# Optimization experiments

Hardware: AMD Instinct MI355X
Metric: run time of the kernel (lower is better)

## Reference

```python
import jax, jax.numpy as jnp
import numpy as np

HEADS = 4
DIM_HEAD = 32


def setup_inputs() -> dict:
    key = jax.random.key(0)
    k1, k2, k3 = jax.random.split(key, 3)
    B, L, D = 16, 8192, 256
    hidden = HEADS * DIM_HEAD  # 128
    x = jax.random.normal(k1, (B, L, D), dtype=jnp.float32)
    W_qkv = jax.random.normal(k2, (D, 3 * hidden), dtype=jnp.float32) * (D ** -0.5)
    W_out = jax.random.normal(k3, (hidden, D), dtype=jnp.float32) * (hidden ** -0.5)
    b_out = jnp.zeros((D,), dtype=jnp.float32)
    return {"x": x, "W_qkv": W_qkv, "W_out": W_out, "b_out": b_out}


def reference(x, W_qkv, W_out, b_out):
    B, L, D = x.shape
    scale = DIM_HEAD ** -0.5
    # 1x1 conv == per-token matmul
    qkv = jnp.einsum('bld,df->blf', x, W_qkv)  # [B, L, 3*h*dh]
    qkv = qkv.reshape(B, L, 3, HEADS, DIM_HEAD)
    q = jnp.transpose(qkv[:, :, 0], (0, 2, 1, 3)) * scale          # [B, h, L, d]
    k = jax.nn.softmax(jnp.transpose(qkv[:, :, 1], (0, 2, 1, 3)), axis=2)  # softmax over L
    v = jnp.transpose(qkv[:, :, 2], (0, 2, 1, 3))                  # [B, h, L, e]
    context = jnp.einsum('bhld,bhle->bhde', k, v)                  # [B, h, d, e]
    out = jnp.einsum('bhde,bhld->bhle', context, q)                # [B, h, L, e]
    out = jnp.transpose(out, (0, 2, 1, 3)).reshape(B, L, HEADS * DIM_HEAD)
    return jnp.einsum('blf,fd->bld', out, W_out) + b_out
```

## Files before the change

### kernel.cpp

```cpp
#include <hip/hip_runtime.h>
#include <math.h>


typedef __attribute__((ext_vector_type(8))) short bf16x8;
typedef __attribute__((ext_vector_type(4))) float f32x4;
typedef __attribute__((ext_vector_type(4))) unsigned u32x4;

__device__ __forceinline__ unsigned cvt_pk2(float a, float b) {
    unsigned r;
    asm("v_cvt_pk_bf16_f32 %0, %1, %2" : "=v"(r) : "v"(a), "v"(b));
    return r;
}
__device__ __forceinline__ ushort bf16_rn(float f) {
    return (ushort)cvt_pk2(f, f);
}
__device__ __forceinline__ float bf16f(ushort h) { return __uint_as_float(((unsigned)h) << 16); }

__device__ __forceinline__ void glds16(const void* g, void* l) {
    __builtin_amdgcn_global_load_lds((const __attribute__((address_space(1))) unsigned int*)g,
                                     (__attribute__((address_space(3))) unsigned int*)l,
                                     16, 0, 0);
}

__global__ __launch_bounds__(256) void prep_kernel(const float* __restrict__ W,
                                                   ushort* __restrict__ wh,
                                                   ushort* __restrict__ wl) {
    int n = blockIdx.x, k = threadIdx.x;
    float f = W[k * 384 + 128 + n];
    ushort h = bf16_rn(f);
    wh[n * 256 + k] = h;
    wl[n * 256 + k] = bf16_rn(f - bf16f(h));
}

__global__ __launch_bounds__(256) void gemm_kv(
    const float* __restrict__ X,
    const ushort* __restrict__ Wh, const ushort* __restrict__ Wl,
    float* __restrict__ S_part, float* __restrict__ Z_part) {
    __shared__ __align__(16) char smem[40960];
    float*  As  = (float*)smem;
    ushort* Bsh = (ushort*)(smem + 8192);
    ushort* Bsl = (ushort*)(smem + 8192 + 16384);
    float*  tile = (float*)smem;

    const int tid = threadIdx.x;
    const int blk = blockIdx.x;
    const long row0 = (long)blk * 64;
    const int lane = tid & 63, wave = tid >> 6;
    const int wc = wave * 64;
    const int m = lane & 15, quad = lane >> 4;
    const int ra = lane >> 3, pa = lane & 7;
    const int rb = lane >> 2, pb = lane & 3;

    f32x4 acc[4][4] = {};

    for (int k0 = 0; k0 < 256; k0 += 32) {
#pragma unroll
        for (int s = 0; s < 2; ++s) {
            int seg = s * 4 + wave;
            int r = seg * 8 + ra;
            int q = pa ^ (r & 7);
            glds16(&X[(row0 + r) * 256 + k0 + q * 4], &As[seg * 256]);
        }
#pragma unroll
        for (int s = 0; s < 4; ++s) {
            int seg = s * 4 + wave;
            int r = seg * 16 + rb;
            int q = pb ^ ((r >> 1) & 3);
            glds16(&Wh[r * 256 + k0 + q * 8], &Bsh[seg * 512]);
            glds16(&Wl[r * 256 + k0 + q * 8], &Bsl[seg * 512]);
        }
        __syncthreads();

        bf16x8 bh[4], bl[4];
#pragma unroll
        for (int j = 0; j < 4; ++j) {
            int r = wc + j * 16 + m;
            int p = quad ^ ((r >> 1) & 3);
            bh[j] = *(const bf16x8*)&Bsh[r * 32 + p * 8];
            bl[j] = *(const bf16x8*)&Bsl[r * 32 + p * 8];
        }
#pragma unroll
        for (int i = 0; i < 4; ++i) {
            int r = i * 16 + m;
            int p0 = (quad * 2) ^ (r & 7);
            int p1 = (quad * 2 + 1) ^ (r & 7);
            f32x4 a0 = *(const f32x4*)&As[r * 32 + p0 * 4];
            f32x4 a1 = *(const f32x4*)&As[r * 32 + p1 * 4];
            u32x4 ahw, alw;
#pragma unroll
            for (int e = 0; e < 2; ++e) {
                float f0 = a0[2 * e], f1 = a0[2 * e + 1];
                unsigned h = cvt_pk2(f0, f1);
                ahw[e] = h;
                alw[e] = cvt_pk2(f0 - __uint_as_float(h << 16),
                                 f1 - __uint_as_float(h & 0xFFFF0000u));
            }
#pragma unroll
            for (int e = 0; e < 2; ++e) {
                float f0 = a1[2 * e], f1 = a1[2 * e + 1];
                unsigned h = cvt_pk2(f0, f1);
                ahw[2 + e] = h;
                alw[2 + e] = cvt_pk2(f0 - __uint_as_float(h << 16),
                                     f1 - __uint_as_float(h & 0xFFFF0000u));
            }
            bf16x8 ah = __builtin_bit_cast(bf16x8, ahw);
            bf16x8 al = __builtin_bit_cast(bf16x8, alw);
#pragma unroll
            for (int j = 0; j < 4; ++j) {
                acc[i][j] = __builtin_amdgcn_mfma_f32_16x16x32_bf16(ah, bh[j], acc[i][j], 0, 0, 0);
                acc[i][j] = __builtin_amdgcn_mfma_f32_16x16x32_bf16(ah, bl[j], acc[i][j], 0, 0, 0);
                acc[i][j] = __builtin_amdgcn_mfma_f32_16x16x32_bf16(al, bh[j], acc[i][j], 0, 0, 0);
            }
        }
        __syncthreads();
    }

    const int h = wave, d = lane >> 1, eg = lane & 1, e0 = eg * 16;
    float sacc[16] = {};
    float z = 0.f;
    for (int half = 0; half < 2; ++half) {
        if (half) __syncthreads();
#pragma unroll
        for (int ii = 0; ii < 2; ++ii) {
            int i = half * 2 + ii;
#pragma unroll
            for (int r4 = 0; r4 < 4; ++r4) {
                int rl = ii * 16 + quad * 4 + r4;
#pragma unroll
                for (int j = 0; j < 4; ++j) {
                    int c = wc + j * 16 + m;
                    float v = acc[i][j][r4];
                    tile[rl * 260 + c] = (c < 128) ? __expf(v) : v;
                }
            }
        }
        __syncthreads();
#pragma unroll 4
        for (int l = 0; l < 32; ++l) {
            const float* rowp = &tile[l * 260];
            float ek = rowp[h * 32 + d];
            const f32x4* vp = (const f32x4*)&rowp[128 + h * 32 + e0];
            f32x4 v0 = vp[0], v1 = vp[1], v2 = vp[2], v3 = vp[3];
            z += ek;
            sacc[0]  += ek * v0[0]; sacc[1]  += ek * v0[1]; sacc[2]  += ek * v0[2]; sacc[3]  += ek * v0[3];
            sacc[4]  += ek * v1[0]; sacc[5]  += ek * v1[1]; sacc[6]  += ek * v1[2]; sacc[7]  += ek * v1[3];
            sacc[8]  += ek * v2[0]; sacc[9]  += ek * v2[1]; sacc[10] += ek * v2[2]; sacc[11] += ek * v2[3];
            sacc[12] += ek * v3[0]; sacc[13] += ek * v3[1]; sacc[14] += ek * v3[2]; sacc[15] += ek * v3[3];
        }
    }
    long sb = (long)blk * 4096 + h * 1024 + d * 32 + e0;
#pragma unroll
    for (int t = 0; t < 16; ++t) S_part[sb + t] = sacc[t];
    if (eg == 0) Z_part[blk * 128 + h * 32 + d] = z;
}

__global__ __launch_bounds__(256) void reduce_parts(const float* __restrict__ Sp,
                                                    const float* __restrict__ Zp,
                                                    float* __restrict__ S,
                                                    float* __restrict__ Z) {
    int g = blockIdx.x * 256 + threadIdx.x;
    int b = g >> 12, idx = g & 4095;
    const float* p = Sp + ((long)b * 128) * 4096 + idx;
    float s0 = 0.f, s1 = 0.f;
#pragma unroll 4
    for (int j = 0; j < 64; ++j) { s0 += p[j * 4096]; s1 += p[(j + 64) * 4096]; }
    S[g] = s0 + s1;
    if (g < 2048) {
        int bb = g >> 7, c = g & 127;
        const float* q = Zp + (long)bb * 128 * 128 + c;
        float z0 = 0.f, z1 = 0.f;
#pragma unroll 4
        for (int j = 0; j < 64; ++j) { z0 += q[j * 128]; z1 += q[(j + 64) * 128]; }
        Z[g] = z0 + z1;
    }
}

__global__ __launch_bounds__(256) void combine_kernel(const float* __restrict__ S,
                                                      const float* __restrict__ Z,
                                                      const float* __restrict__ Wout,
                                                      float* __restrict__ m2f) {
    int bh = blockIdx.x;
    int b = bh >> 2, h = bh & 3;
    int n = threadIdx.x;
    __shared__ float ctx[32][33];
    __shared__ float zs[32];
    if (n < 32) zs[n] = Z[b * 128 + h * 32 + n];
    __syncthreads();
#pragma unroll
    for (int t = 0; t < 4; ++t) {
        int idx = t * 256 + n;
        ctx[idx >> 5][idx & 31] = S[(long)b * 4096 + h * 1024 + idx] / zs[idx >> 5];
    }
    __syncthreads();
    const float scale = 0.17677669529663687f;
    float acc[32];
#pragma unroll
    for (int dd = 0; dd < 32; ++dd) acc[dd] = 0.f;
    for (int e = 0; e < 32; ++e) {
        float w = Wout[(h * 32 + e) * 256 + n];
#pragma unroll
        for (int dd = 0; dd < 32; ++dd) acc[dd] += ctx[dd][e] * w;
    }
#pragma unroll
    for (int dd = 0; dd < 32; ++dd)
        m2f[((long)(b * 128 + h * 32 + dd)) * 256 + n] = acc[dd] * scale;
}

__global__ __launch_bounds__(256) void w2eff_kernel(const float* __restrict__ Wqkv,
                                                    const float* __restrict__ m2f,
                                                    ushort* __restrict__ w2h,
                                                    ushort* __restrict__ w2l) {
    int bid = blockIdx.x;
    int b = bid >> 4, kg = bid & 15;
    int n = threadIdx.x;
    __shared__ float lWq[16 * 128];
#pragma unroll
    for (int u = 0; u < 8; ++u) {
        int idx = u * 256 + n;
        int k = idx >> 7, hd = idx & 127;
        lWq[idx] = Wqkv[(kg * 16 + k) * 384 + hd];
    }
    __syncthreads();
    float acc[16] = {};
    for (int hd = 0; hd < 128; ++hd) {
        float mm = m2f[((long)(b * 128 + hd)) * 256 + n];
#pragma unroll
        for (int k = 0; k < 16; ++k) acc[k] += lWq[k * 128 + hd] * mm;
    }
    long base = ((long)(b * 256 + n)) * 256 + kg * 16;
#pragma unroll
    for (int k = 0; k < 16; ++k) {
        ushort hh = bf16_rn(acc[k]);
        w2h[base + k] = hh;
        w2l[base + k] = bf16_rn(acc[k] - bf16f(hh));
    }
}

__global__ __launch_bounds__(256) void gemm2_kernel(
    const float* __restrict__ X,
    const ushort* __restrict__ W2h, const ushort* __restrict__ W2l,
    const float* __restrict__ bias, float* __restrict__ out) {
    __shared__ __align__(16) float  As[4096];
    __shared__ __align__(16) ushort Bsh[4096];
    __shared__ __align__(16) ushort Bsl[4096];
    const int tid = threadIdx.x;
    const int wg = blockIdx.x;
    const int xcd = wg & 7;
    const int u = wg >> 3;
    const int cbl = u & 1;
    const int gid = (u >> 1) * 8 + xcd;
    const long bz = gid >> 6;
    const int row0 = (gid & 63) * 128;
    const int col0 = cbl * 128;
    const float* Xb = X + bz * (8192L * 256);
    const ushort* Bh = W2h + bz * (256L * 256);
    const ushort* Bl = W2l + bz * (256L * 256);
    const int lane = tid & 63, wave = tid >> 6;
    const int wr = (wave & 1) * 64, wc = (wave >> 1) * 64;
    const int m = lane & 15, quad = lane >> 4;
    const int ra = lane >> 3, pa = lane & 7;
    const int rb = lane >> 2, pb = lane & 3;

    f32x4 acc[4][4] = {};

    for (int k0 = 0; k0 < 256; k0 += 32) {
#pragma unroll
        for (int s = 0; s < 4; ++s) {
            int seg = s * 4 + wave;
            int r = seg * 8 + ra;
            int q = pa ^ (r & 7);
            glds16(&Xb[(long)(row0 + r) * 256 + k0 + q * 4], &As[seg * 256]);
        }
#pragma unroll
        for (int s = 0; s < 2; ++s) {
            int seg = s * 4 + wave;
            int r = seg * 16 + rb;
            int q = pb ^ ((r >> 1) & 3);
            glds16(&Bh[(col0 + r) * 256 + k0 + q * 8], &Bsh[seg * 512]);
            glds16(&Bl[(col0 + r) * 256 + k0 + q * 8], &Bsl[seg * 512]);
        }
        __syncthreads();

        bf16x8 bh[4], bl[4];
#pragma unroll
        for (int j = 0; j < 4; ++j) {
            int r = wc + j * 16 + m;
            int p = quad ^ ((r >> 1) & 3);
            bh[j] = *(const bf16x8*)&Bsh[r * 32 + p * 8];
            bl[j] = *(const bf16x8*)&Bsl[r * 32 + p * 8];
        }
#pragma unroll
        for (int i = 0; i < 4; ++i) {
            int r = wr + i * 16 + m;
            int p0 = (quad * 2) ^ (r & 7);
            int p1 = (quad * 2 + 1) ^ (r & 7);
            f32x4 a0 = *(const f32x4*)&As[r * 32 + p0 * 4];
            f32x4 a1 = *(const f32x4*)&As[r * 32 + p1 * 4];
            u32x4 ahw, alw;
#pragma unroll
            for (int e = 0; e < 2; ++e) {
                float f0 = a0[2 * e], f1 = a0[2 * e + 1];
                unsigned h = cvt_pk2(f0, f1);
                ahw[e] = h;
                alw[e] = cvt_pk2(f0 - __uint_as_float(h << 16),
                                 f1 - __uint_as_float(h & 0xFFFF0000u));
            }
#pragma unroll
            for (int e = 0; e < 2; ++e) {
                float f0 = a1[2 * e], f1 = a1[2 * e + 1];
                unsigned h = cvt_pk2(f0, f1);
                ahw[2 + e] = h;
                alw[2 + e] = cvt_pk2(f0 - __uint_as_float(h << 16),
                                     f1 - __uint_as_float(h & 0xFFFF0000u));
            }
            bf16x8 ah = __builtin_bit_cast(bf16x8, ahw);
            bf16x8 al = __builtin_bit_cast(bf16x8, alw);
#pragma unroll
            for (int j = 0; j < 4; ++j) {
                acc[i][j] = __builtin_amdgcn_mfma_f32_16x16x32_bf16(ah, bh[j], acc[i][j], 0, 0, 0);
                acc[i][j] = __builtin_amdgcn_mfma_f32_16x16x32_bf16(ah, bl[j], acc[i][j], 0, 0, 0);
                acc[i][j] = __builtin_amdgcn_mfma_f32_16x16x32_bf16(al, bh[j], acc[i][j], 0, 0, 0);
            }
        }
        __syncthreads();
    }

    float bv[4];
#pragma unroll
    for (int j = 0; j < 4; ++j) bv[j] = bias[col0 + wc + j * 16 + m];
    float* outb = out + bz * (8192L * 256);
#pragma unroll
    for (int i = 0; i < 4; ++i)
#pragma unroll
        for (int r4 = 0; r4 < 4; ++r4) {
            long row = row0 + wr + i * 16 + quad * 4 + r4;
#pragma unroll
            for (int j = 0; j < 4; ++j)
                outb[row * 256 + col0 + wc + j * 16 + m] = acc[i][j][r4] + bv[j];
        }
}

extern "C" void kernel_launch(void* const* d_in, const int* in_sizes, int n_in,
                              void* d_out, int out_size, void* d_ws, size_t ws_size,
                              hipStream_t stream) {
    const float* x     = (const float*)d_in[0];
    const float* W_qkv = (const float*)d_in[1];
    const float* W_out = (const float*)d_in[2];
    const float* b_out = (const float*)d_in[3];
    float* out = (float*)d_out;

    char* p = (char*)d_ws;
    ushort* wth = (ushort*)p; p += 256 * 256 * 2;
    ushort* wtl = (ushort*)p; p += 256 * 256 * 2;
    float* Sp   = (float*)p;  p += (long)2048 * 4096 * 4;
    float* Zp   = (float*)p;  p += 2048 * 128 * 4;
    float* Sr   = (float*)p;  p += 16 * 4096 * 4;
    float* Zr   = (float*)p;  p += 2048 * 4;
    float* m2f  = (float*)p;  p += 16 * 128 * 256 * 4;
    ushort* w2h = (ushort*)p; p += (long)16 * 256 * 256 * 2;
    ushort* w2l = (ushort*)p; p += (long)16 * 256 * 256 * 2;

    prep_kernel<<<256, 256, 0, stream>>>(W_qkv, wth, wtl);
    gemm_kv<<<2048, 256, 0, stream>>>(x, wth, wtl, Sp, Zp);
    reduce_parts<<<256, 256, 0, stream>>>(Sp, Zp, Sr, Zr);
    combine_kernel<<<64, 256, 0, stream>>>(Sr, Zr, W_out, m2f);
    w2eff_kernel<<<256, 256, 0, stream>>>(W_qkv, m2f, w2h, w2l);
    gemm2_kernel<<<2048, 256, 0, stream>>>(x, w2h, w2l, b_out, out);
}
```

Measured before the change: 388.5 us.

## Use single bf16 pass for K/V GEMM and pre-split X once in LDS

The K/V projection GEMM drops the three-pass split-bf16 scheme and uses one plain bf16 MFMA pass, so the low-part weight buffer and its prep are removed. X is loaded into registers, converted to bf16, and written to LDS in bf16 form. In the output GEMM, X is split into hi/lo bf16 once per tile while staging into LDS, instead of every wave re-converting the fp32 fragments it reads. This cuts MFMA count and conversion work, but the K/V path now carries bf16 rounding error into the softmax over L and the context.

```diff
diff --git a/kernel.cpp b/kernel.cpp
--- a/kernel.cpp
+++ b/kernel.cpp
@@ -23,23 +23,18 @@
 }
 
 __global__ __launch_bounds__(256) void prep_kernel(const float* __restrict__ W,
-                                                   ushort* __restrict__ wh,
-                                                   ushort* __restrict__ wl) {
+                                                   ushort* __restrict__ wh) {
     int n = blockIdx.x, k = threadIdx.x;
-    float f = W[k * 384 + 128 + n];
-    ushort h = bf16_rn(f);
-    wh[n * 256 + k] = h;
-    wl[n * 256 + k] = bf16_rn(f - bf16f(h));
+    wh[n * 256 + k] = bf16_rn(W[k * 384 + 128 + n]);
 }
 
 __global__ __launch_bounds__(256) void gemm_kv(
     const float* __restrict__ X,
-    const ushort* __restrict__ Wh, const ushort* __restrict__ Wl,
+    const ushort* __restrict__ Wh,
     float* __restrict__ S_part, float* __restrict__ Z_part) {
-    __shared__ __align__(16) char smem[40960];
-    float*  As  = (float*)smem;
-    ushort* Bsh = (ushort*)(smem + 8192);
-    ushort* Bsl = (ushort*)(smem + 8192 + 16384);
+    __shared__ __align__(16) char smem[33280];
+    ushort* Ash = (ushort*)smem;
+    ushort* Bsh = (ushort*)(smem + 4096);
     float*  tile = (float*)smem;
 
     const int tid = threadIdx.x;
@@ -48,70 +43,47 @@
     const int lane = tid & 63, wave = tid >> 6;
     const int wc = wave * 64;
     const int m = lane & 15, quad = lane >> 4;
-    const int ra = lane >> 3, pa = lane & 7;
     const int rb = lane >> 2, pb = lane & 3;
+    const int rA = tid >> 2, qA = tid & 3;
+    const int pA = qA ^ ((rA >> 1) & 3);
 
     f32x4 acc[4][4] = {};
 
     for (int k0 = 0; k0 < 256; k0 += 32) {
-#pragma unroll
-        for (int s = 0; s < 2; ++s) {
-            int seg = s * 4 + wave;
-            int r = seg * 8 + ra;
-            int q = pa ^ (r & 7);
-            glds16(&X[(row0 + r) * 256 + k0 + q * 4], &As[seg * 256]);
-        }
+        const float* xp = &X[(row0 + rA) * 256 + k0 + qA * 8];
+        f32x4 x0 = *(const f32x4*)xp;
+        f32x4 x1 = *(const f32x4*)(xp + 4);
 #pragma unroll
         for (int s = 0; s < 4; ++s) {
             int seg = s * 4 + wave;
             int r = seg * 16 + rb;
             int q = pb ^ ((r >> 1) & 3);
             glds16(&Wh[r * 256 + k0 + q * 8], &Bsh[seg * 512]);
-            glds16(&Wl[r * 256 + k0 + q * 8], &Bsl[seg * 512]);
-        }
-        __syncthreads();
-
-        bf16x8 bh[4], bl[4];
+        }
+        u32x4 aw;
+        aw[0] = cvt_pk2(x0[0], x0[1]); aw[1] = cvt_pk2(x0[2], x0[3]);
+        aw[2] = cvt_pk2(x1[0], x1[1]); aw[3] = cvt_pk2(x1[2], x1[3]);
+        *(u32x4*)&Ash[rA * 32 + pA * 8] = aw;
+        __syncthreads();
+
+        bf16x8 bh[4], av[4];
 #pragma unroll
         for (int j = 0; j < 4; ++j) {
             int r = wc + j * 16 + m;
             int p = quad ^ ((r >> 1) & 3);
             bh[j] = *(const bf16x8*)&Bsh[r * 32 + p * 8];
-            bl[j] = *(const bf16x8*)&Bsl[r * 32 + p * 8];
         }
 #pragma unroll
         for (int i = 0; i < 4; ++i) {
             int r = i * 16 + m;
-            int p0 = (quad * 2) ^ (r & 7);
-            int p1 = (quad * 2 + 1) ^ (r & 7);
-            f32x4 a0 = *(const f32x4*)&As[r * 32 + p0 * 4];
-            f32x4 a1 = *(const f32x4*)&As[r * 32 + p1 * 4];
-            u32x4 ahw, alw;
-#pragma unroll
-            for (int e = 0; e < 2; ++e) {
-                float f0 = a0[2 * e], f1 = a0[2 * e + 1];
-                unsigned h = cvt_pk2(f0, f1);
-                ahw[e] = h;
-                alw[e] = cvt_pk2(f0 - __uint_as_float(h << 16),
-                                 f1 - __uint_as_float(h & 0xFFFF0000u));
-            }
-#pragma unroll
-            for (int e = 0; e < 2; ++e) {
-                float f0 = a1[2 * e], f1 = a1[2 * e + 1];
-                unsigned h = cvt_pk2(f0, f1);
-                ahw[2 + e] = h;
-                alw[2 + e] = cvt_pk2(f0 - __uint_as_float(h << 16),
-                                     f1 - __uint_as_float(h & 0xFFFF0000u));
-            }
-            bf16x8 ah = __builtin_bit_cast(bf16x8, ahw);
-            bf16x8 al = __builtin_bit_cast(bf16x8, alw);
-#pragma unroll
-            for (int j = 0; j < 4; ++j) {
-                acc[i][j] = __builtin_amdgcn_mfma_f32_16x16x32_bf16(ah, bh[j], acc[i][j], 0, 0, 0);
-                acc[i][j] = __builtin_amdgcn_mfma_f32_16x16x32_bf16(ah, bl[j], acc[i][j], 0, 0, 0);
-                acc[i][j] = __builtin_amdgcn_mfma_f32_16x16x32_bf16(al, bh[j], acc[i][j], 0, 0, 0);
-            }
-        }
+            int p = quad ^ ((r >> 1) & 3);
+            av[i] = *(const bf16x8*)&Ash[r * 32 + p * 8];
+        }
+#pragma unroll
+        for (int i = 0; i < 4; ++i)
+#pragma unroll
+            for (int j = 0; j < 4; ++j)
+                acc[i][j] = __builtin_amdgcn_mfma_f32_16x16x32_bf16(av[i], bh[j], acc[i][j], 0, 0, 0);
         __syncthreads();
     }
 
@@ -240,7 +212,8 @@
     const float* __restrict__ X,
     const ushort* __restrict__ W2h, const ushort* __restrict__ W2l,
     const float* __restrict__ bias, float* __restrict__ out) {
-    __shared__ __align__(16) float  As[4096];
+    __shared__ __align__(16) ushort Ash[4096];
+    __shared__ __align__(16) ushort Asl[4096];
     __shared__ __align__(16) ushort Bsh[4096];
     __shared__ __align__(16) ushort Bsl[4096];
     const int tid = threadIdx.x;
@@ -258,18 +231,19 @@
     const int lane = tid & 63, wave = tid >> 6;
     const int wr = (wave & 1) * 64, wc = (wave >> 1) * 64;
     const int m = lane & 15, quad = lane >> 4;
-    const int ra = lane >> 3, pa = lane & 7;
     const int rb = lane >> 2, pb = lane & 3;
 
     f32x4 acc[4][4] = {};
 
     for (int k0 = 0; k0 < 256; k0 += 32) {
-#pragma unroll
-        for (int s = 0; s < 4; ++s) {
-            int seg = s * 4 + wave;
-            int r = seg * 8 + ra;
-            int q = pa ^ (r & 7);
-            glds16(&Xb[(long)(row0 + r) * 256 + k0 + q * 4], &As[seg * 256]);
+        f32x4 xv[2][2];
+#pragma unroll
+        for (int t = 0; t < 2; ++t) {
+            int uu = t * 256 + tid;
+            int r = uu >> 2, q = uu & 3;
+            const float* xp = &Xb[(long)(row0 + r) * 256 + k0 + q * 8];
+            xv[t][0] = *(const f32x4*)xp;
+            xv[t][1] = *(const f32x4*)(xp + 4);
         }
 #pragma unroll
         for (int s = 0; s < 2; ++s) {
@@ -279,49 +253,53 @@
             glds16(&Bh[(col0 + r) * 256 + k0 + q * 8], &Bsh[seg * 512]);
             glds16(&Bl[(col0 + r) * 256 + k0 + q * 8], &Bsl[seg * 512]);
         }
-        __syncthreads();
-
-        bf16x8 bh[4], bl[4];
-#pragma unroll
-        for (int j = 0; j < 4; ++j) {
-            int r = wc + j * 16 + m;
-            int p = quad ^ ((r >> 1) & 3);
-            bh[j] = *(const bf16x8*)&Bsh[r * 32 + p * 8];
-            bl[j] = *(const bf16x8*)&Bsl[r * 32 + p * 8];
-        }
+#pragma unroll
+        for (int t = 0; t < 2; ++t) {
+            int uu = t * 256 + tid;
+            int r = uu >> 2, q = uu & 3;
+            int p = q ^ ((r >> 1) & 3);
+            u32x4 hw, lw;
+#pragma unroll
+            for (int e = 0; e < 2; ++e) {
+                float f0 = xv[t][0][2 * e], f1 = xv[t][0][2 * e + 1];
+                unsigned hh = cvt_pk2(f0, f1);
+                hw[e] = hh;
+                lw[e] = cvt_pk2(f0 - __uint_as_float(hh << 16),
+                                f1 - __uint_as_float(hh & 0xFFFF0000u));
+            }
+#pragma unroll
+            for (int e = 0; e < 2; ++e) {
+                float f0 = xv[t][1][2 * e], f1 = xv[t][1][2 * e + 1];
+                unsigned hh = cvt_pk2(f0, f1);
+                hw[2 + e] = hh;
+                lw[2 + e] = cvt_pk2(f0 - __uint_as_float(hh << 16),
+                                    f1 - __uint_as_float(hh & 0xFFFF0000u));
+            }
+            *(u32x4*)&Ash[r * 32 + p * 8] = hw;
+            *(u32x4*)&Asl[r * 32 + p * 8] = lw;
+        }
+        __syncthreads();
+
+        bf16x8 af[2][4], bg[2][4];
 #pragma unroll
         for (int i = 0; i < 4; ++i) {
-            int r = wr + i * 16 + m;
-            int p0 = (quad * 2) ^ (r & 7);
-            int p1 = (quad * 2 + 1) ^ (r & 7);
-            f32x4 a0 = *(const f32x4*)&As[r * 32 + p0 * 4];
-            f32x4 a1 = *(const f32x4*)&As[r * 32 + p1 * 4];
-            u32x4 ahw, alw;
-#pragma unroll
-            for (int e = 0; e < 2; ++e) {
-                float f0 = a0[2 * e], f1 = a0[2 * e + 1];
-                unsigned h = cvt_pk2(f0, f1);
-                ahw[e] = h;
-                alw[e] = cvt_pk2(f0 - __uint_as_float(h << 16),
-                                 f1 - __uint_as_float(h & 0xFFFF0000u));
+            int rA = wr + i * 16 + m;
+            int pA = quad ^ ((rA >> 1) & 3);
+            af[0][i] = *(const bf16x8*)&Ash[rA * 32 + pA * 8];
+            af[1][i] = *(const bf16x8*)&Asl[rA * 32 + pA * 8];
+            int rB = wc + i * 16 + m;
+            int pB = quad ^ ((rB >> 1) & 3);
+            bg[0][i] = *(const bf16x8*)&Bsh[rB * 32 + pB * 8];
+            bg[1][i] = *(const bf16x8*)&Bsl[rB * 32 + pB * 8];
+        }
+#pragma unroll
+        for (int i = 0; i < 4; ++i)
+#pragma unroll
+            for (int j = 0; j < 4; ++j) {
+                acc[i][j] = __builtin_amdgcn_mfma_f32_16x16x32_bf16(af[0][i], bg[0][j], acc[i][j], 0, 0, 0);
+                acc[i][j] = __builtin_amdgcn_mfma_f32_16x16x32_bf16(af[0][i], bg[1][j], acc[i][j], 0, 0, 0);
+                acc[i][j] = __builtin_amdgcn_mfma_f32_16x16x32_bf16(af[1][i], bg[0][j], acc[i][j], 0, 0, 0);
             }
-#pragma unroll
-            for (int e = 0; e < 2; ++e) {
-                float f0 = a1[2 * e], f1 = a1[2 * e + 1];
-                unsigned h = cvt_pk2(f0, f1);
-                ahw[2 + e] = h;
-                alw[2 + e] = cvt_pk2(f0 - __uint_as_float(h << 16),
-                                     f1 - __uint_as_float(h & 0xFFFF0000u));
-            }
-            bf16x8 ah = __builtin_bit_cast(bf16x8, ahw);
-            bf16x8 al = __builtin_bit_cast(bf16x8, alw);
-#pragma unroll
-            for (int j = 0; j < 4; ++j) {
-                acc[i][j] = __builtin_amdgcn_mfma_f32_16x16x32_bf16(ah, bh[j], acc[i][j], 0, 0, 0);
-                acc[i][j] = __builtin_amdgcn_mfma_f32_16x16x32_bf16(ah, bl[j], acc[i][j], 0, 0, 0);
-                acc[i][j] = __builtin_amdgcn_mfma_f32_16x16x32_bf16(al, bh[j], acc[i][j], 0, 0, 0);
-            }
-        }
         __syncthreads();
     }
 
@@ -351,7 +329,6 @@
 
     char* p = (char*)d_ws;
     ushort* wth = (ushort*)p; p += 256 * 256 * 2;
-    ushort* wtl = (ushort*)p; p += 256 * 256 * 2;
     float* Sp   = (float*)p;  p += (long)2048 * 4096 * 4;
     float* Zp   = (float*)p;  p += 2048 * 128 * 4;
     float* Sr   = (float*)p;  p += 16 * 4096 * 4;
@@ -360,8 +337,8 @@
     ushort* w2h = (ushort*)p; p += (long)16 * 256 * 256 * 2;
     ushort* w2l = (ushort*)p; p += (long)16 * 256 * 256 * 2;
 
-    prep_kernel<<<256, 256, 0, stream>>>(W_qkv, wth, wtl);
-    gemm_kv<<<2048, 256, 0, stream>>>(x, wth, wtl, Sp, Zp);
+    prep_kernel<<<256, 256, 0, stream>>>(W_qkv, wth);
+    gemm_kv<<<2048, 256, 0, stream>>>(x, wth, Sp, Zp);
     reduce_parts<<<256, 256, 0, stream>>>(Sp, Zp, Sr, Zr);
     combine_kernel<<<64, 256, 0, stream>>>(Sr, Zr, W_out, m2f);
     w2eff_kernel<<<256, 256, 0, stream>>>(W_qkv, m2f, w2h, w2l);
```

Result: faster. 355.9 us (-8.4%).
